# Kernel tuning notes

Hardware: AMD Instinct MI355X
Metric: run time of the kernel (lower is better)

Reference implementation:

```python
import jax, jax.numpy as jnp
import numpy as np

N_USERS = 100000
N_ITEMS = 50000
D = 64
NNZ = 4_800_000
N_HOPS = 3


def setup_inputs() -> dict:
    key = jax.random.key(0)
    k1, k2, k3, k4, k5 = jax.random.split(key, 5)
    n_nodes = N_USERS + N_ITEMS
    user_embed = jax.random.normal(k1, (N_USERS, D), dtype=jnp.float32) * 0.1
    item_embed = jax.random.normal(k2, (N_ITEMS, D), dtype=jnp.float32) * 0.1
    # COO indices of the symmetric-normalized interaction adjacency
    row = jax.random.randint(k3, (NNZ,), 0, n_nodes, dtype=jnp.int32)
    col = jax.random.randint(k4, (NNZ,), 0, n_nodes, dtype=jnp.int32)
    # normalized adjacency values ~ 1/deg scale
    vals = jax.random.uniform(k5, (NNZ,), dtype=jnp.float32) * (1.0 / 32.0)
    return {"user_embed": user_embed, "item_embed": item_embed,
            "row": row, "col": col, "vals": vals}


def reference(user_embed, item_embed, row, col, vals):
    """GraphConv.forward with perturbed=False (path used in M4.forward).

    torch.sparse.mm(A, X) over COO == segment_sum(vals * X[col], row).
    """
    n_users = user_embed.shape[0]
    n_nodes = n_users + item_embed.shape[0]
    ego = jnp.concatenate([user_embed, item_embed], axis=0)  # [N, D]

    def spmm(x):
        return jax.ops.segment_sum(vals[:, None] * x[col], row,
                                   num_segments=n_nodes)

    hop_outs = []
    for _ in range(N_HOPS):
        ego = spmm(ego)
        hop_outs.append(ego)
    layer_embeddings = hop_outs[0]  # k == 0 hop (layer_cl path)
    all_embeddings = jnp.mean(jnp.stack(hop_outs, axis=1), axis=1)  # [N, D]

    return (all_embeddings[:n_users], all_embeddings[n_users:],
            layer_embeddings[:n_users], layer_embeddings[n_users:])
```

## Files before the change

kernel.cpp:

```cpp
#include <hip/hip_runtime.h>
#include <hip/hip_bf16.h>


#define D 64
typedef unsigned short u16;

#define NBP   512
#define TILE  2048
#define FCAP  4608

__device__ __forceinline__ float bf2f(u16 h) {
    union { unsigned int u; float f; } c;
    c.u = ((unsigned int)h) << 16;
    return c.f;
}
__device__ __forceinline__ u16 f2bf(float f) {
    union { float f; unsigned int u; } c; c.f = f;
    unsigned int r = c.u + 0x7FFFu + ((c.u >> 16) & 1u);
    return (u16)(r >> 16);
}

struct U4 { u16 a, b, c, d; } __attribute__((aligned(8)));

__global__ void detect_kernel(const u16* __restrict__ emb,
                              const u16* __restrict__ vals,
                              int* __restrict__ flags) {
    int lane = threadIdx.x;
    int se = 0, sv = 0;
    for (int k = 0; k < 16; ++k) {
        int idx = (lane * 16 + k) * 2;
        u16 he = emb[idx];
        int ee = (he >> 7) & 0xFF;
        if (ee >= 100 && ee < 127) se++;
        u16 hv = vals[idx];
        int ev = (hv >> 7) & 0xFF;
        if ((hv >> 15) == 0 && ev >= 60 && ev < 123) sv++;
    }
    atomicAdd(&flags[0], se);
    atomicAdd(&flags[1], sv);
}

__global__ __launch_bounds__(256)
void convert_kernel(const void* __restrict__ ue, const void* __restrict__ ie,
                    const int* __restrict__ flags, u16* __restrict__ x0,
                    int total, int usz) {
    int i = (blockIdx.x * blockDim.x + threadIdx.x) * 4;
    if (i >= total) return;
    const void* src = (i < usz) ? ue : ie;
    int off = (i < usz) ? i : i - usz;
    U4 o;
    if (flags[0] >= 512) {
        o = *(const U4*)((const u16*)src + off);
    } else {
        const float4 v = *(const float4*)((const float*)src + off);
        o.a = f2bf(v.x); o.b = f2bf(v.y); o.c = f2bf(v.z); o.d = f2bf(v.w);
    }
    *(U4*)(x0 + i) = o;
}

__global__ __launch_bounds__(256)
void bhist_kernel(const int* __restrict__ row, int* __restrict__ bcnt, int nnz) {
    __shared__ int h[NBP];
    int t = threadIdx.x;
    h[t] = 0; h[t + 256] = 0;
    __syncthreads();
    for (int i = blockIdx.x * 256 + t; i < nnz; i += gridDim.x * 256)
        atomicAdd(&h[row[i] >> 9], 1);
    __syncthreads();
    if (h[t])       atomicAdd(&bcnt[t],       h[t]);
    if (h[t + 256]) atomicAdd(&bcnt[t + 256], h[t + 256]);
}

__global__ void bscan_kernel(const int* __restrict__ bcnt, int* __restrict__ bbase,
                             int* __restrict__ bcursor, int nb, int nnz) {
    __shared__ int buf[NBP];
    int t = threadIdx.x;
    int v = (t < nb) ? bcnt[t] : 0;
    buf[t] = v;
    __syncthreads();
    for (int off = 1; off < NBP; off <<= 1) {
        int y = (t >= off) ? buf[t - off] : 0;
        __syncthreads();
        buf[t] += y;
        __syncthreads();
    }
    int excl = buf[t] - v;
    bbase[t] = excl;
    bcursor[t] = excl;
    if (t == 0) bbase[nb] = nnz;
}

__global__ __launch_bounds__(256)
void coarse_kernel(const int* __restrict__ row, const int* __restrict__ col,
                   const void* __restrict__ vals, const int* __restrict__ flags,
                   int* __restrict__ bcursor, int2* __restrict__ es2, int nnz) {
    __shared__ int2 ebuf[TILE];
    __shared__ u16  slotb[TILE];
    __shared__ int  hcnt[NBP], hscn[NBP], goff[NBP];
    int t = threadIdx.x;
    int base = blockIdx.x * TILE;
    int tcnt = nnz - base; if (tcnt > TILE) tcnt = TILE;
    bool vbf = (flags[1] >= 512);

    hcnt[t] = 0; hcnt[t + 256] = 0;
    __syncthreads();

    int eb[8], er[8], ep[8], ev[8];
#pragma unroll
    for (int k = 0; k < 8; ++k) {
        int i = base + k * 256 + t;
        eb[k] = -1;
        if (k * 256 + t < tcnt) {
            int r = row[i];
            int c = col[i];
            float v = vbf ? bf2f(((const u16*)vals)[i]) : ((const float*)vals)[i];
            eb[k] = r >> 9;
            ep[k] = ((r & 511) << 18) | c;
            ev[k] = __float_as_int(v);
            er[k] = atomicAdd(&hcnt[eb[k]], 1);
        }
    }
    __syncthreads();
    hscn[t] = hcnt[t]; hscn[t + 256] = hcnt[t + 256];
    __syncthreads();
    for (int off = 1; off < NBP; off <<= 1) {
        int a0 = (t >= off) ? hscn[t - off] : 0;
        int a1 = (t + 256 >= off) ? hscn[t + 256 - off] : 0;
        __syncthreads();
        hscn[t] += a0; hscn[t + 256] += a1;
        __syncthreads();
    }
#pragma unroll
    for (int k = 0; k < 8; ++k) {
        if (eb[k] >= 0) {
            int slot = hscn[eb[k]] - hcnt[eb[k]] + er[k];
            ebuf[slot] = make_int2(ep[k], ev[k]);
            slotb[slot] = (u16)eb[k];
        }
    }
    __syncthreads();
    if (hcnt[t] > 0)       goff[t]       = atomicAdd(&bcursor[t],       hcnt[t]);
    if (hcnt[t + 256] > 0) goff[t + 256] = atomicAdd(&bcursor[t + 256], hcnt[t + 256]);
    __syncthreads();
#pragma unroll
    for (int k = 0; k < 8; ++k) {
        int p = k * 256 + t;
        if (p < tcnt) {
            int b = slotb[p];
            int dest = goff[b] + (p - (hscn[b] - hcnt[b]));
            es2[dest] = ebuf[p];
        }
    }
}

__global__ __launch_bounds__(256)
void fine_kernel(const int2* __restrict__ es2, const int* __restrict__ bbase,
                 int2* __restrict__ es, int* __restrict__ rp, int n, int nnz) {
    __shared__ int2 obuf[FCAP];
    __shared__ int hist[512], scn[512], cur[128];
    int b = blockIdx.x >> 2, q = blockIdx.x & 3, t = threadIdx.x;
    int r0 = b * 512;
    int s = bbase[b], e = bbase[b + 1];
    if (b == 0 && q == 0 && t == 0) rp[n] = nnz;

    hist[t] = 0; hist[t + 256] = 0;
    __syncthreads();
    for (int i = s + t; i < e; i += 256)
        atomicAdd(&hist[(unsigned)es2[i].x >> 18], 1);
    __syncthreads();
    scn[t] = hist[t]; scn[t + 256] = hist[t + 256];
    __syncthreads();
    for (int off = 1; off < 512; off <<= 1) {
        int a0 = (t >= off) ? scn[t - off] : 0;
        int a1 = (t + 256 >= off) ? scn[t + 256 - off] : 0;
        __syncthreads();
        scn[t] += a0; scn[t + 256] += a1;
        __syncthreads();
    }
    int qbase = q * 128;
    int q0 = qbase ? scn[qbase - 1] : 0;
    int qcnt = scn[qbase + 127] - q0;
    int ds = s + q0;

    if (t < 128) {
        int rl = qbase + t;
        int r  = r0 + rl;
        int ex = scn[rl] - hist[rl];
        if (r < n) rp[r] = s + ex;
        cur[t] = (qcnt <= FCAP) ? (ex - q0) : (s + ex);
    }
    __syncthreads();

    if (qcnt <= FCAP) {
        for (int i = s + t; i < e; i += 256) {
            int2 p = es2[i];
            int rl = (unsigned)p.x >> 18;
            if ((rl >> 7) == q) {
                int pos = atomicAdd(&cur[rl & 127], 1);
                obuf[pos] = make_int2(p.x & 0x3FFFF, p.y);
            }
        }
        __syncthreads();
        for (int p = t; p < qcnt; p += 256)
            es[ds + p] = obuf[p];
    } else {
        for (int i = s + t; i < e; i += 256) {
            int2 p = es2[i];
            int rl = (unsigned)p.x >> 18;
            if ((rl >> 7) == q) {
                int pos = atomicAdd(&cur[rl & 127], 1);
                es[pos] = make_int2(p.x & 0x3FFFF, p.y);
            }
        }
    }
}


__global__ __launch_bounds__(256)
void spmm_kernel(const u16* __restrict__ x, u16* __restrict__ y,
                 const int* __restrict__ rp, const int2* __restrict__ es, int n) {
    int wid  = (blockIdx.x * blockDim.x + threadIdx.x) >> 6;
    int lane = threadIdx.x & 63;
    int qt   = lane >> 4;
    int sub  = lane & 15;
    int r    = (wid << 2) + qt;
    int e = 0, e1 = 0;
    if (r < n) { e = rp[r]; e1 = rp[r + 1]; }
    const u16* xs = x + (sub << 2);

    float a0 = 0.f, a1 = 0.f, a2 = 0.f, a3 = 0.f;
    float b0 = 0.f, b1 = 0.f, b2 = 0.f, b3 = 0.f;

    for (; e + 8 <= e1; e += 8) {
        int2 p0 = es[e],     p1 = es[e + 1], p2 = es[e + 2], p3 = es[e + 3];
        int2 p4 = es[e + 4], p5 = es[e + 5], p6 = es[e + 6], p7 = es[e + 7];
        U4 v0 = *(const U4*)(xs + (p0.x << 6));
        U4 v1 = *(const U4*)(xs + (p1.x << 6));
        U4 v2 = *(const U4*)(xs + (p2.x << 6));
        U4 v3 = *(const U4*)(xs + (p3.x << 6));
        U4 v4 = *(const U4*)(xs + (p4.x << 6));
        U4 v5 = *(const U4*)(xs + (p5.x << 6));
        U4 v6 = *(const U4*)(xs + (p6.x << 6));
        U4 v7 = *(const U4*)(xs + (p7.x << 6));
        float w0 = __int_as_float(p0.y), w1 = __int_as_float(p1.y);
        float w2 = __int_as_float(p2.y), w3 = __int_as_float(p3.y);
        float w4 = __int_as_float(p4.y), w5 = __int_as_float(p5.y);
        float w6 = __int_as_float(p6.y), w7 = __int_as_float(p7.y);
        a0 += w0 * bf2f(v0.a); a1 += w0 * bf2f(v0.b); a2 += w0 * bf2f(v0.c); a3 += w0 * bf2f(v0.d);
        b0 += w1 * bf2f(v1.a); b1 += w1 * bf2f(v1.b); b2 += w1 * bf2f(v1.c); b3 += w1 * bf2f(v1.d);
        a0 += w2 * bf2f(v2.a); a1 += w2 * bf2f(v2.b); a2 += w2 * bf2f(v2.c); a3 += w2 * bf2f(v2.d);
        b0 += w3 * bf2f(v3.a); b1 += w3 * bf2f(v3.b); b2 += w3 * bf2f(v3.c); b3 += w3 * bf2f(v3.d);
        a0 += w4 * bf2f(v4.a); a1 += w4 * bf2f(v4.b); a2 += w4 * bf2f(v4.c); a3 += w4 * bf2f(v4.d);
        b0 += w5 * bf2f(v5.a); b1 += w5 * bf2f(v5.b); b2 += w5 * bf2f(v5.c); b3 += w5 * bf2f(v5.d);
        a0 += w6 * bf2f(v6.a); a1 += w6 * bf2f(v6.b); a2 += w6 * bf2f(v6.c); a3 += w6 * bf2f(v6.d);
        b0 += w7 * bf2f(v7.a); b1 += w7 * bf2f(v7.b); b2 += w7 * bf2f(v7.c); b3 += w7 * bf2f(v7.d);
    }
    for (; e < e1; ++e) {
        int2 p = es[e];
        U4 v = *(const U4*)(xs + (p.x << 6));
        float w = __int_as_float(p.y);
        a0 += w * bf2f(v.a); a1 += w * bf2f(v.b); a2 += w * bf2f(v.c); a3 += w * bf2f(v.d);
    }
    if (r < n) {
        U4 o;
        o.a = f2bf(a0 + b0); o.b = f2bf(a1 + b1);
        o.c = f2bf(a2 + b2); o.d = f2bf(a3 + b3);
        *(U4*)(y + (r << 6) + (sub << 2)) = o;
    }
}

__global__ __launch_bounds__(256)
void spmm_last_kernel(const u16* __restrict__ x2, const u16* __restrict__ x1,
                      float* __restrict__ out,
                      const int* __restrict__ rp, const int2* __restrict__ es, int n) {
    int wid  = (blockIdx.x * blockDim.x + threadIdx.x) >> 6;
    int lane = threadIdx.x & 63;
    int qt   = lane >> 4;
    int sub  = lane & 15;
    int r    = (wid << 2) + qt;
    int e = 0, e1 = 0;
    if (r < n) { e = rp[r]; e1 = rp[r + 1]; }
    const u16* xs = x2 + (sub << 2);

    float a0 = 0.f, a1 = 0.f, a2 = 0.f, a3 = 0.f;
    float b0 = 0.f, b1 = 0.f, b2 = 0.f, b3 = 0.f;

    for (; e + 8 <= e1; e += 8) {
        int2 p0 = es[e],     p1 = es[e + 1], p2 = es[e + 2], p3 = es[e + 3];
        int2 p4 = es[e + 4], p5 = es[e + 5], p6 = es[e + 6], p7 = es[e + 7];
        U4 v0 = *(const U4*)(xs + (p0.x << 6));
        U4 v1 = *(const U4*)(xs + (p1.x << 6));
        U4 v2 = *(const U4*)(xs + (p2.x << 6));
        U4 v3 = *(const U4*)(xs + (p3.x << 6));
        U4 v4 = *(const U4*)(xs + (p4.x << 6));
        U4 v5 = *(const U4*)(xs + (p5.x << 6));
        U4 v6 = *(const U4*)(xs + (p6.x << 6));
        U4 v7 = *(const U4*)(xs + (p7.x << 6));
        float w0 = __int_as_float(p0.y), w1 = __int_as_float(p1.y);
        float w2 = __int_as_float(p2.y), w3 = __int_as_float(p3.y);
        float w4 = __int_as_float(p4.y), w5 = __int_as_float(p5.y);
        float w6 = __int_as_float(p6.y), w7 = __int_as_float(p7.y);
        a0 += w0 * bf2f(v0.a); a1 += w0 * bf2f(v0.b); a2 += w0 * bf2f(v0.c); a3 += w0 * bf2f(v0.d);
        b0 += w1 * bf2f(v1.a); b1 += w1 * bf2f(v1.b); b2 += w1 * bf2f(v1.c); b3 += w1 * bf2f(v1.d);
        a0 += w2 * bf2f(v2.a); a1 += w2 * bf2f(v2.b); a2 += w2 * bf2f(v2.c); a3 += w2 * bf2f(v2.d);
        b0 += w3 * bf2f(v3.a); b1 += w3 * bf2f(v3.b); b2 += w3 * bf2f(v3.c); b3 += w3 * bf2f(v3.d);
        a0 += w4 * bf2f(v4.a); a1 += w4 * bf2f(v4.b); a2 += w4 * bf2f(v4.c); a3 += w4 * bf2f(v4.d);
        b0 += w5 * bf2f(v5.a); b1 += w5 * bf2f(v5.b); b2 += w5 * bf2f(v5.c); b3 += w5 * bf2f(v5.d);
        a0 += w6 * bf2f(v6.a); a1 += w6 * bf2f(v6.b); a2 += w6 * bf2f(v6.c); a3 += w6 * bf2f(v6.d);
        b0 += w7 * bf2f(v7.a); b1 += w7 * bf2f(v7.b); b2 += w7 * bf2f(v7.c); b3 += w7 * bf2f(v7.d);
    }
    for (; e < e1; ++e) {
        int2 p = es[e];
        U4 v = *(const U4*)(xs + (p.x << 6));
        float w = __int_as_float(p.y);
        a0 += w * bf2f(v.a); a1 += w * bf2f(v.b); a2 += w * bf2f(v.c); a3 += w * bf2f(v.d);
    }
    if (r < n) {
        int idx = (r << 6) + (sub << 2);
        U4 h1v = *(const U4*)(x1 + idx);
        U4 h2v = *(const U4*)(x2 + idx);
        float h1a = bf2f(h1v.a), h1b = bf2f(h1v.b), h1c = bf2f(h1v.c), h1d = bf2f(h1v.d);
        float h2a = bf2f(h2v.a), h2b = bf2f(h2v.b), h2c = bf2f(h2v.c), h2d = bf2f(h2v.d);
        float4 o;
        o.x = (h1a + h2a + (a0 + b0)) * (1.0f / 3.0f);
        o.y = (h1b + h2b + (a1 + b1)) * (1.0f / 3.0f);
        o.z = (h1c + h2c + (a2 + b2)) * (1.0f / 3.0f);
        o.w = (h1d + h2d + (a3 + b3)) * (1.0f / 3.0f);
        *(float4*)(out + idx) = o;
        float4 l;
        l.x = h1a; l.y = h1b; l.z = h1c; l.w = h1d;
        *(float4*)(out + (size_t)n * D + idx) = l;
    }
}


extern "C" void kernel_launch(void* const* d_in, const int* in_sizes, int n_in,
                              void* d_out, int out_size, void* d_ws, size_t ws_size,
                              hipStream_t stream) {
    const void* ue   = d_in[0];
    const void* ie   = d_in[1];
    const int*  row  = (const int*)d_in[2];
    const int*  col  = (const int*)d_in[3];
    const void* vals = d_in[4];

    const int nu  = in_sizes[0] / D;
    const int ni  = in_sizes[1] / D;
    const int n   = nu + ni;
    const int nnz = in_sizes[2];

    char* ws = (char*)d_ws;
    u16*  X0     = (u16*)ws;   ws += (size_t)n * D * sizeof(u16);
    u16*  X1     = (u16*)ws;   ws += (size_t)n * D * sizeof(u16);
    u16*  X2     = (u16*)ws;   ws += (size_t)n * D * sizeof(u16);
    int2* es2    = (int2*)X1;
    int2* es     = (int2*)ws;  ws += (size_t)nnz * sizeof(int2);
    int*  rp     = (int*)ws;   ws += (size_t)(n + 1) * sizeof(int);
    int*  bcnt   = (int*)ws;   ws += NBP * sizeof(int);
    int*  flags  = (int*)ws;   ws += 2 * sizeof(int);
    int*  bbase  = (int*)ws;   ws += (NBP + 1) * sizeof(int);
    int*  bcursor= (int*)ws;   ws += NBP * sizeof(int);

    const int tb = 256;
    const int rblocks = (n + 15) / 16;
    const int cblocks = (n * D / 4 + tb - 1) / tb;
    const int NB      = (n + 511) / 512;
    const int coarseb = (nnz + TILE - 1) / TILE;

    hipMemsetAsync(bcnt, 0, (NBP + 2) * sizeof(int), stream);
    detect_kernel <<<1, 64, 0, stream>>>((const u16*)ue, (const u16*)vals, flags);
    convert_kernel<<<cblocks, tb, 0, stream>>>(ue, ie, flags, X0, n * D, nu * D);
    bhist_kernel  <<<512, tb, 0, stream>>>(row, bcnt, nnz);
    bscan_kernel  <<<1, NBP, 0, stream>>>(bcnt, bbase, bcursor, NB, nnz);
    coarse_kernel <<<coarseb, tb, 0, stream>>>(row, col, vals, flags, bcursor, es2, nnz);
    fine_kernel   <<<NB * 4, tb, 0, stream>>>(es2, bbase, es, rp, n, nnz);

    spmm_kernel     <<<rblocks, tb, 0, stream>>>(X0, X1, rp, es, n);
    spmm_kernel     <<<rblocks, tb, 0, stream>>>(X1, X2, rp, es, n);
    spmm_last_kernel<<<rblocks, tb, 0, stream>>>(X2, X1, (float*)d_out, rp, es, n);
}
```

Before: 641.1 us.

## Use 128-row coarse buckets so fine sort reads each bucket once

The two-pass COO-to-CSR bucket sort now uses 128-row buckets (2048 buckets) instead of 512-row ones. Each fine block handles a whole bucket, stages it in LDS and scatters it directly, instead of four blocks each rescanning a 512-row bucket and keeping a quarter. The scans in bscan and coarse are rewritten as per-thread serial segments plus a block scan, and the goff array is folded into hcnt. This removes the 4x redundant reading of es2 in the fine pass, at the cost of more global cursor atomics and a wider LDS histogram in the coarse pass.

Result: slower. 866.9 us (+35.2%).

```diff
diff --git a/kernel.cpp b/kernel.cpp
--- a/kernel.cpp
+++ b/kernel.cpp
@@ -5,7 +5,8 @@
 #define D 64
 typedef unsigned short u16;
 
-#define NBP   512
+#define NBP   2048
+#define BSH   7
 #define TILE  2048
 #define FCAP  4608
 
@@ -62,31 +63,48 @@
 void bhist_kernel(const int* __restrict__ row, int* __restrict__ bcnt, int nnz) {
     __shared__ int h[NBP];
     int t = threadIdx.x;
-    h[t] = 0; h[t + 256] = 0;
+#pragma unroll
+    for (int j = 0; j < NBP / 256; ++j) h[t + j * 256] = 0;
     __syncthreads();
     for (int i = blockIdx.x * 256 + t; i < nnz; i += gridDim.x * 256)
-        atomicAdd(&h[row[i] >> 9], 1);
-    __syncthreads();
-    if (h[t])       atomicAdd(&bcnt[t],       h[t]);
-    if (h[t + 256]) atomicAdd(&bcnt[t + 256], h[t + 256]);
+        atomicAdd(&h[row[i] >> BSH], 1);
+    __syncthreads();
+#pragma unroll
+    for (int j = 0; j < NBP / 256; ++j) {
+        int b = t + j * 256;
+        if (h[b]) atomicAdd(&bcnt[b], h[b]);
+    }
 }
 
 __global__ void bscan_kernel(const int* __restrict__ bcnt, int* __restrict__ bbase,
                              int* __restrict__ bcursor, int nb, int nnz) {
-    __shared__ int buf[NBP];
+    __shared__ int wsum[512];
     int t = threadIdx.x;
-    int v = (t < nb) ? bcnt[t] : 0;
-    buf[t] = v;
-    __syncthreads();
-    for (int off = 1; off < NBP; off <<= 1) {
-        int y = (t >= off) ? buf[t - off] : 0;
-        __syncthreads();
-        buf[t] += y;
-        __syncthreads();
-    }
-    int excl = buf[t] - v;
-    bbase[t] = excl;
-    bcursor[t] = excl;
+    int v[4], l[4];
+    int acc = 0;
+#pragma unroll
+    for (int k = 0; k < 4; ++k) {
+        int i = t * 4 + k;
+        v[k] = (i < nb) ? bcnt[i] : 0;
+        acc += v[k];
+        l[k] = acc;
+    }
+    wsum[t] = acc;
+    __syncthreads();
+    for (int off = 1; off < 512; off <<= 1) {
+        int a = (t >= off) ? wsum[t - off] : 0;
+        __syncthreads();
+        wsum[t] += a;
+        __syncthreads();
+    }
+    int base = wsum[t] - acc;
+#pragma unroll
+    for (int k = 0; k < 4; ++k) {
+        int i = t * 4 + k;
+        int excl = base + l[k] - v[k];
+        bbase[i] = excl;
+        bcursor[i] = excl;
+    }
     if (t == 0) bbase[nb] = nnz;
 }
 
@@ -96,13 +114,15 @@
                    int* __restrict__ bcursor, int2* __restrict__ es2, int nnz) {
     __shared__ int2 ebuf[TILE];
     __shared__ u16  slotb[TILE];
-    __shared__ int  hcnt[NBP], hscn[NBP], goff[NBP];
+    __shared__ int  hcnt[NBP], hscn[NBP];
+    __shared__ int  wsum[256];
     int t = threadIdx.x;
     int base = blockIdx.x * TILE;
     int tcnt = nnz - base; if (tcnt > TILE) tcnt = TILE;
     bool vbf = (flags[1] >= 512);
 
-    hcnt[t] = 0; hcnt[t + 256] = 0;
+#pragma unroll
+    for (int j = 0; j < NBP / 256; ++j) hcnt[t + j * 256] = 0;
     __syncthreads();
 
     int eb[8], er[8], ep[8], ev[8];
@@ -114,22 +134,31 @@
             int r = row[i];
             int c = col[i];
             float v = vbf ? bf2f(((const u16*)vals)[i]) : ((const float*)vals)[i];
-            eb[k] = r >> 9;
-            ep[k] = ((r & 511) << 18) | c;
+            eb[k] = r >> BSH;
+            ep[k] = ((r & 127) << 18) | c;
             ev[k] = __float_as_int(v);
             er[k] = atomicAdd(&hcnt[eb[k]], 1);
         }
     }
     __syncthreads();
-    hscn[t] = hcnt[t]; hscn[t + 256] = hcnt[t + 256];
-    __syncthreads();
-    for (int off = 1; off < NBP; off <<= 1) {
-        int a0 = (t >= off) ? hscn[t - off] : 0;
-        int a1 = (t + 256 >= off) ? hscn[t + 256 - off] : 0;
-        __syncthreads();
-        hscn[t] += a0; hscn[t + 256] += a1;
-        __syncthreads();
-    }
+    int a = 0, lo[8];
+#pragma unroll
+    for (int k = 0; k < 8; ++k) {
+        a += hcnt[t * 8 + k];
+        lo[k] = a;
+    }
+    wsum[t] = a;
+    __syncthreads();
+    for (int off = 1; off < 256; off <<= 1) {
+        int x = (t >= off) ? wsum[t - off] : 0;
+        __syncthreads();
+        wsum[t] += x;
+        __syncthreads();
+    }
+    int tp = wsum[t] - a;
+#pragma unroll
+    for (int k = 0; k < 8; ++k) hscn[t * 8 + k] = tp + lo[k];
+    __syncthreads();
 #pragma unroll
     for (int k = 0; k < 8; ++k) {
         if (eb[k] >= 0) {
@@ -139,16 +168,22 @@
         }
     }
     __syncthreads();
-    if (hcnt[t] > 0)       goff[t]       = atomicAdd(&bcursor[t],       hcnt[t]);
-    if (hcnt[t + 256] > 0) goff[t + 256] = atomicAdd(&bcursor[t + 256], hcnt[t + 256]);
+#pragma unroll
+    for (int k = 0; k < 8; ++k) {
+        int b = t * 8 + k;
+        int c = hcnt[b];
+        if (c > 0) {
+            int g = atomicAdd(&bcursor[b], c);
+            hcnt[b] = g - (hscn[b] - c);
+        }
+    }
     __syncthreads();
 #pragma unroll
     for (int k = 0; k < 8; ++k) {
         int p = k * 256 + t;
         if (p < tcnt) {
             int b = slotb[p];
-            int dest = goff[b] + (p - (hscn[b] - hcnt[b]));
-            es2[dest] = ebuf[p];
+            es2[hcnt[b] + p] = ebuf[p];
         }
     }
 }
@@ -157,60 +192,56 @@
 void fine_kernel(const int2* __restrict__ es2, const int* __restrict__ bbase,
                  int2* __restrict__ es, int* __restrict__ rp, int n, int nnz) {
     __shared__ int2 obuf[FCAP];
-    __shared__ int hist[512], scn[512], cur[128];
-    int b = blockIdx.x >> 2, q = blockIdx.x & 3, t = threadIdx.x;
-    int r0 = b * 512;
+    __shared__ int hist[128], scn[128], cur[128];
+    int b = blockIdx.x, t = threadIdx.x;
+    int r0 = b << BSH;
     int s = bbase[b], e = bbase[b + 1];
-    if (b == 0 && q == 0 && t == 0) rp[n] = nnz;
-
-    hist[t] = 0; hist[t + 256] = 0;
-    __syncthreads();
-    for (int i = s + t; i < e; i += 256)
-        atomicAdd(&hist[(unsigned)es2[i].x >> 18], 1);
-    __syncthreads();
-    scn[t] = hist[t]; scn[t + 256] = hist[t + 256];
-    __syncthreads();
-    for (int off = 1; off < 512; off <<= 1) {
-        int a0 = (t >= off) ? scn[t - off] : 0;
-        int a1 = (t + 256 >= off) ? scn[t + 256 - off] : 0;
-        __syncthreads();
-        scn[t] += a0; scn[t + 256] += a1;
-        __syncthreads();
-    }
-    int qbase = q * 128;
-    int q0 = qbase ? scn[qbase - 1] : 0;
-    int qcnt = scn[qbase + 127] - q0;
-    int ds = s + q0;
-
-    if (t < 128) {
-        int rl = qbase + t;
-        int r  = r0 + rl;
-        int ex = scn[rl] - hist[rl];
-        if (r < n) rp[r] = s + ex;
-        cur[t] = (qcnt <= FCAP) ? (ex - q0) : (s + ex);
-    }
-    __syncthreads();
-
-    if (qcnt <= FCAP) {
+    int cnt = e - s;
+    if (b == 0 && t == 0) rp[n] = nnz;
+
+    if (t < 128) hist[t] = 0;
+    __syncthreads();
+    bool fit = (cnt <= FCAP);
+    if (fit) {
         for (int i = s + t; i < e; i += 256) {
             int2 p = es2[i];
-            int rl = (unsigned)p.x >> 18;
-            if ((rl >> 7) == q) {
-                int pos = atomicAdd(&cur[rl & 127], 1);
-                obuf[pos] = make_int2(p.x & 0x3FFFF, p.y);
-            }
-        }
-        __syncthreads();
-        for (int p = t; p < qcnt; p += 256)
-            es[ds + p] = obuf[p];
+            obuf[i - s] = p;
+            atomicAdd(&hist[(unsigned)p.x >> 18], 1);
+        }
+    } else {
+        for (int i = s + t; i < e; i += 256)
+            atomicAdd(&hist[(unsigned)es2[i].x >> 18], 1);
+    }
+    __syncthreads();
+    if (t < 128) scn[t] = hist[t];
+    __syncthreads();
+    for (int off = 1; off < 128; off <<= 1) {
+        int a = (t < 128 && t >= off) ? scn[t - off] : 0;
+        __syncthreads();
+        if (t < 128) scn[t] += a;
+        __syncthreads();
+    }
+    if (t < 128) {
+        int ex = scn[t] - hist[t];
+        int r = r0 + t;
+        if (r < n) rp[r] = s + ex;
+        cur[t] = s + ex;
+    }
+    __syncthreads();
+
+    if (fit) {
+        for (int p = t; p < cnt; p += 256) {
+            int2 v = obuf[p];
+            int rl = (unsigned)v.x >> 18;
+            int pos = atomicAdd(&cur[rl], 1);
+            es[pos] = make_int2(v.x & 0x3FFFF, v.y);
+        }
     } else {
         for (int i = s + t; i < e; i += 256) {
-            int2 p = es2[i];
-            int rl = (unsigned)p.x >> 18;
-            if ((rl >> 7) == q) {
-                int pos = atomicAdd(&cur[rl & 127], 1);
-                es[pos] = make_int2(p.x & 0x3FFFF, p.y);
-            }
+            int2 v = es2[i];
+            int rl = (unsigned)v.x >> 18;
+            int pos = atomicAdd(&cur[rl], 1);
+            es[pos] = make_int2(v.x & 0x3FFFF, v.y);
         }
     }
 }
@@ -363,16 +394,16 @@
     const int tb = 256;
     const int rblocks = (n + 15) / 16;
     const int cblocks = (n * D / 4 + tb - 1) / tb;
-    const int NB      = (n + 511) / 512;
+    const int NB      = (n + 127) / 128;
     const int coarseb = (nnz + TILE - 1) / TILE;
 
     hipMemsetAsync(bcnt, 0, (NBP + 2) * sizeof(int), stream);
     detect_kernel <<<1, 64, 0, stream>>>((const u16*)ue, (const u16*)vals, flags);
     convert_kernel<<<cblocks, tb, 0, stream>>>(ue, ie, flags, X0, n * D, nu * D);
     bhist_kernel  <<<512, tb, 0, stream>>>(row, bcnt, nnz);
-    bscan_kernel  <<<1, NBP, 0, stream>>>(bcnt, bbase, bcursor, NB, nnz);
+    bscan_kernel  <<<1, 512, 0, stream>>>(bcnt, bbase, bcursor, NB, nnz);
     coarse_kernel <<<coarseb, tb, 0, stream>>>(row, col, vals, flags, bcursor, es2, nnz);
-    fine_kernel   <<<NB * 4, tb, 0, stream>>>(es2, bbase, es, rp, n, nnz);
+    fine_kernel   <<<NB, tb, 0, stream>>>(es2, bbase, es, rp, n, nnz);
 
     spmm_kernel     <<<rblocks, tb, 0, stream>>>(X0, X1, rp, es, n);
     spmm_kernel     <<<rblocks, tb, 0, stream>>>(X1, X2, rp, es, n);
```
